# Optimization experiments

Hardware: AMD Instinct MI355X
Metric: run time of the kernel (lower is better)

Reference implementation:

```python
import jax, jax.numpy as jnp
import numpy as np

# Qwen3-0.6B-like config; 4 equal-length requests flattened into [R*S, H]
L, R, S, H = 2, 4, 1024, 1024
NH, NKV, DH = 16, 8, 128
FF = 3072
EPS = 1e-6
THETA = 1e6
SCALE = 0.02  # weight init scale to keep activations sane


def setup_inputs() -> dict:
    key = jax.random.key(0)
    ks = jax.random.split(key, 8)
    return {
        "hidden_states": jax.random.normal(ks[0], (R * S, H), jnp.float32),
        "Wq": jax.random.normal(ks[1], (L, H, NH * DH), jnp.float32) * SCALE,
        "Wk": jax.random.normal(ks[2], (L, H, NKV * DH), jnp.float32) * SCALE,
        "Wv": jax.random.normal(ks[3], (L, H, NKV * DH), jnp.float32) * SCALE,
        "Wo": jax.random.normal(ks[4], (L, NH * DH, H), jnp.float32) * SCALE,
        "q_norm_w": jnp.ones((L, DH), jnp.float32),
        "k_norm_w": jnp.ones((L, DH), jnp.float32),
        "ln1_w": jnp.ones((L, H), jnp.float32),
        "ln2_w": jnp.ones((L, H), jnp.float32),
        "Wg": jax.random.normal(ks[5], (L, H, FF), jnp.float32) * SCALE,
        "Wu": jax.random.normal(ks[6], (L, H, FF), jnp.float32) * SCALE,
        "Wd": jax.random.normal(ks[7], (L, FF, H), jnp.float32) * SCALE,
        "final_norm_w": jnp.ones((H,), jnp.float32),
    }


def _rms(x, w):
    return x * jax.lax.rsqrt(jnp.mean(x * x, axis=-1, keepdims=True) + EPS) * w


def _rope_tables():
    inv_freq = 1.0 / (THETA ** (jnp.arange(0, DH, 2, dtype=jnp.float32) / DH))
    pos = jnp.arange(S, dtype=jnp.float32)  # per-request positions 0..S-1 (prefill)
    freqs = pos[:, None] * inv_freq[None, :]        # [S, DH/2]
    emb = jnp.concatenate([freqs, freqs], axis=-1)  # [S, DH]
    return jnp.cos(emb), jnp.sin(emb)


def _rotate_half(x):
    x1, x2 = jnp.split(x, 2, axis=-1)
    return jnp.concatenate([-x2, x1], axis=-1)


def _apply_rope(x, cos, sin):
    # x: [R, heads, S, DH]; cos/sin: [S, DH]
    c = cos[None, None]
    s = sin[None, None]
    return x * c + _rotate_half(x) * s


def reference(hidden_states, Wq, Wk, Wv, Wo, q_norm_w, k_norm_w, ln1_w, ln2_w,
              Wg, Wu, Wd, final_norm_w):
    cos, sin = _rope_tables()
    causal = jnp.tril(jnp.ones((S, S), dtype=bool))  # per-request causal mask
    neg = jnp.finfo(hidden_states.dtype).min
    scaling = 1.0 / jnp.sqrt(jnp.asarray(DH, hidden_states.dtype))

    x = hidden_states
    for l in range(L):
        # --- attention block ---
        residual = x
        h = _rms(x, ln1_w[l])                       # [R*S, H]
        q = (h @ Wq[l]).reshape(R, S, NH, DH)
        k = (h @ Wk[l]).reshape(R, S, NKV, DH)
        v = (h @ Wv[l]).reshape(R, S, NKV, DH)
        q = _rms(q, q_norm_w[l]).transpose(0, 2, 1, 3)   # [R, NH, S, DH]
        k = _rms(k, k_norm_w[l]).transpose(0, 2, 1, 3)   # [R, NKV, S, DH]
        v = v.transpose(0, 2, 1, 3)                      # [R, NKV, S, DH]
        q = _apply_rope(q, cos, sin)
        k = _apply_rope(k, cos, sin)
        # GQA: repeat KV heads
        rep = NH // NKV
        k = jnp.repeat(k, rep, axis=1)
        v = jnp.repeat(v, rep, axis=1)
        scores = jnp.einsum('rhqd,rhkd->rhqk', q, k) * scaling
        scores = jnp.where(causal[None, None], scores, neg)
        attn = jax.nn.softmax(scores, axis=-1)
        o = jnp.einsum('rhqk,rhkd->rhqd', attn, v)       # [R, NH, S, DH]
        o = o.transpose(0, 2, 1, 3).reshape(R * S, NH * DH)
        x = residual + o @ Wo[l]
        # --- MLP block ---
        residual = x
        h = _rms(x, ln2_w[l])
        x = residual + (jax.nn.silu(h @ Wg[l]) * (h @ Wu[l])) @ Wd[l]
    return _rms(x, final_norm_w)
```

## Files before the change

### kernel.cpp

```cpp
#include <hip/hip_runtime.h>
#include <hip/hip_bf16.h>

typedef __bf16 bf16;
typedef __bf16 bf16x8 __attribute__((ext_vector_type(8)));
typedef float f32x4 __attribute__((ext_vector_type(4)));

#define DEVINL __device__ __forceinline__
#define SBAR() asm volatile("s_barrier" ::: "memory")

constexpr int L_ = 2, R_ = 4, S_ = 1024, H_ = 1024;
constexpr int NH_ = 16, NKV_ = 8, DH_ = 128;
constexpr int FF_ = 3072;
constexpr int T_ = R_ * S_;

DEVINL void gload16(const bf16* g, bf16* l) {
    __builtin_amdgcn_global_load_lds(
        (const __attribute__((address_space(1))) void*)g,
        (__attribute__((address_space(3))) void*)l, 16, 0, 0);
}

__global__ void rope_tables_kernel(float* __restrict__ cosb, float* __restrict__ sinb) {
    int s = blockIdx.x;
    int i = threadIdx.x;
    float inv = __expf(-(float)i * (1.0f / 64.0f) * 13.815510557964274f);
    float f = (float)s * inv;
    cosb[s * 64 + i] = cosf(f);
    sinb[s * 64 + i] = sinf(f);
}

template <bool OUT_BF16>
__global__ __launch_bounds__(256) void rmsnorm_kernel(const float* __restrict__ x,
                                                      const float* __restrict__ w,
                                                      void* __restrict__ out) {
    int row = blockIdx.x;
    const float* xr = x + (size_t)row * H_;
    int t = threadIdx.x;
    float v[4];
    float ss = 0.f;
#pragma unroll
    for (int j = 0; j < 4; ++j) {
        v[j] = xr[t + 256 * j];
        ss += v[j] * v[j];
    }
#pragma unroll
    for (int off = 32; off; off >>= 1) ss += __shfl_xor(ss, off);
    __shared__ float part[4];
    if ((t & 63) == 0) part[t >> 6] = ss;
    __syncthreads();
    ss = part[0] + part[1] + part[2] + part[3];
    float r = rsqrtf(ss * (1.0f / (float)H_) + 1e-6f);
#pragma unroll
    for (int j = 0; j < 4; ++j) {
        int c = t + 256 * j;
        float o = v[j] * r * w[c];
        if constexpr (OUT_BF16)
            ((bf16*)out)[(size_t)row * H_ + c] = (bf16)o;
        else
            ((float*)out)[(size_t)row * H_ + c] = o;
    }
}

__global__ __launch_bounds__(256) void transpose_all_kernel(
    const float* __restrict__ Wq, const float* __restrict__ Wk, const float* __restrict__ Wv,
    const float* __restrict__ Wo, const float* __restrict__ Wg, const float* __restrict__ Wu,
    const float* __restrict__ Wd, bf16* __restrict__ wqkv_t, bf16* __restrict__ wo_t,
    bf16* __restrict__ wgu_t, bf16* __restrict__ wd_t) {
    __shared__ float tile[32][33];
    int bid = blockIdx.x;
    const float* in;
    bf16* out;
    int Rk, Cn, mode, tid;
    if (bid < 2048) { in = Wq; out = wqkv_t; Rk = 1024; Cn = 2048; mode = 0; tid = bid; }
    else if (bid < 3072) { in = Wk; out = wqkv_t + (size_t)2048 * 1024; Rk = 1024; Cn = 1024; mode = 0; tid = bid - 2048; }
    else if (bid < 4096) { in = Wv; out = wqkv_t + (size_t)3072 * 1024; Rk = 1024; Cn = 1024; mode = 0; tid = bid - 3072; }
    else if (bid < 6144) { in = Wo; out = wo_t; Rk = 2048; Cn = 1024; mode = 0; tid = bid - 4096; }
    else if (bid < 9216) { in = Wg; out = wgu_t; Rk = 1024; Cn = 3072; mode = 1; tid = bid - 6144; }
    else if (bid < 12288) { in = Wu; out = wgu_t; Rk = 1024; Cn = 3072; mode = 2; tid = bid - 9216; }
    else { in = Wd; out = wd_t; Rk = 3072; Cn = 1024; mode = 0; tid = bid - 12288; }
    int nbx = Cn >> 5;
    int c0 = (tid % nbx) * 32, r0 = (tid / nbx) * 32;
    int t = threadIdx.x;
    int tc = t & 31, tr = t >> 5;
#pragma unroll
    for (int i = 0; i < 4; ++i) {
        int r = tr + i * 8;
        tile[r][tc] = in[(size_t)(r0 + r) * Cn + c0 + tc];
    }
    __syncthreads();
#pragma unroll
    for (int i = 0; i < 4; ++i) {
        int c = c0 + tr + i * 8;
        int n = (mode == 0) ? c : (((c >> 4) << 5) + ((mode == 2) ? 16 : 0) + (c & 15));
        out[(size_t)n * Rk + r0 + tc] = (bf16)tile[tc][tr + i * 8];
    }
}

__global__ __launch_bounds__(256) void vt_kernel(const bf16* __restrict__ qkv,
                                                 bf16* __restrict__ vt) {
    __shared__ bf16 tile[32][34];
    int s0 = blockIdx.x * 32, c0 = blockIdx.y * 32, r = blockIdx.z;
    int t = threadIdx.x, tc = t & 31, tr = t >> 5;
#pragma unroll
    for (int i = 0; i < 4; ++i) {
        int s = tr + i * 8;
        tile[s][tc] = qkv[(size_t)(r * 1024 + s0 + s) * 4096 + 3072 + c0 + tc];
    }
    __syncthreads();
#pragma unroll
    for (int i = 0; i < 4; ++i) {
        int c = tr + i * 8;
        vt[((size_t)(r * 1024 + c0 + c)) * 1024 + s0 + tc] = tile[tc][c];
    }
}

template <int EPI>
__global__ __launch_bounds__(512, 2) void gemmQ_kernel(const bf16* __restrict__ A,
                                                       const bf16* __restrict__ Bt,
                                                       void* __restrict__ out,
                                                       int M, int N, int K) {
    __shared__ bf16 lds[49152];
    const int NT = K >> 5;
    int nbm = M >> 8, nbn = N >> 8;
    int slice = nbn >> 3;
    int id = blockIdx.x;
    int xcd = id & 7, wi = id >> 3;
    int bm = (wi % nbm) << 8, bn = (xcd * slice + wi / nbm) << 8;
    int t = threadIdx.x, lane = t & 63, w = t >> 6;
    int wm = w >> 2, wn = w & 3;
    int hi = lane >> 4, f = lane & 15;

    int srow = t >> 2;
    int ssc = (t & 3) ^ ((srow >> 1) & 3);
    const bf16* a0 = A + (size_t)(bm + srow) * K + (ssc << 3);
    const bf16* a1 = A + (size_t)(bm + 128 + srow) * K + (ssc << 3);
    const bf16* b0 = Bt + (size_t)(bn + srow) * K + (ssc << 3);
    const bf16* b1 = Bt + (size_t)(bn + 128 + srow) * K + (ssc << 3);

    f32x4 acc[8][4] = {};

    gload16(a0, lds + 0 * 8192 + w * 512);
    gload16(a1, lds + 0 * 8192 + 4096 + w * 512);
    gload16(b0, lds + 24576 + 0 * 8192 + w * 512);
    gload16(b1, lds + 24576 + 0 * 8192 + 4096 + w * 512);
    gload16(a0 + 32, lds + 1 * 8192 + w * 512);
    gload16(a1 + 32, lds + 1 * 8192 + 4096 + w * 512);
    gload16(b0 + 32, lds + 24576 + 1 * 8192 + w * 512);
    gload16(b1 + 32, lds + 24576 + 1 * 8192 + 4096 + w * 512);
    asm volatile("s_waitcnt vmcnt(4)" ::: "memory");
    SBAR();

    int cb = 0;
    for (int tau = 0; tau < NT; ++tau) {
        const bf16* aB = lds + cb * 8192;
        const bf16* bB = lds + 24576 + cb * 8192;
        int sb = (cb == 0) ? 2 : cb - 1;
        bool doStage = (tau + 2 < NT);
        int tt = tau + 2;

        bf16x8 af[4], bfv[4];
#pragma unroll
        for (int mf = 0; mf < 4; ++mf) {
            int row = wm * 128 + mf * 16 + f;
            af[mf] = *(const bf16x8*)(aB + row * 32 + ((hi ^ ((row >> 1) & 3)) << 3));
        }
#pragma unroll
        for (int nf = 0; nf < 4; ++nf) {
            int row = wn * 64 + nf * 16 + f;
            bfv[nf] = *(const bf16x8*)(bB + row * 32 + ((hi ^ ((row >> 1) & 3)) << 3));
        }
        if (doStage) {
            gload16(a0 + tt * 32, lds + sb * 8192 + w * 512);
            gload16(a1 + tt * 32, lds + sb * 8192 + 4096 + w * 512);
        }
        SBAR();
        __builtin_amdgcn_s_setprio(1);
#pragma unroll
        for (int mf = 0; mf < 4; ++mf)
#pragma unroll
            for (int nf = 0; nf < 4; ++nf)
                acc[mf][nf] = __builtin_amdgcn_mfma_f32_16x16x32_bf16(af[mf], bfv[nf],
                                                                      acc[mf][nf], 0, 0, 0);
        __builtin_amdgcn_s_setprio(0);
        SBAR();

        bf16x8 af2[4];
#pragma unroll
        for (int mf = 0; mf < 4; ++mf) {
            int row = wm * 128 + (mf + 4) * 16 + f;
            af2[mf] = *(const bf16x8*)(aB + row * 32 + ((hi ^ ((row >> 1) & 3)) << 3));
        }
        if (doStage) {
            gload16(b0 + tt * 32, lds + 24576 + sb * 8192 + w * 512);
            gload16(b1 + tt * 32, lds + 24576 + sb * 8192 + 4096 + w * 512);
        }
        SBAR();
        __builtin_amdgcn_s_setprio(1);
#pragma unroll
        for (int mf = 0; mf < 4; ++mf)
#pragma unroll
            for (int nf = 0; nf < 4; ++nf)
                acc[mf + 4][nf] = __builtin_amdgcn_mfma_f32_16x16x32_bf16(af2[mf], bfv[nf],
                                                                          acc[mf + 4][nf], 0, 0, 0);
        __builtin_amdgcn_s_setprio(0);
        if (tau < NT - 2)
            asm volatile("s_waitcnt vmcnt(4)" ::: "memory");
        else
            asm volatile("s_waitcnt vmcnt(0)" ::: "memory");
        SBAR();
        cb = (cb == 2) ? 0 : cb + 1;
    }

    int rb = bm + wm * 128 + hi * 4;
#pragma unroll
    for (int mf = 0; mf < 8; ++mf) {
        if constexpr (EPI == 5) {
#pragma unroll
            for (int p = 0; p < 2; ++p) {
                int col = ((bn + wn * 64) >> 1) + p * 16 + f;
#pragma unroll
                for (int g = 0; g < 4; ++g) {
                    float gv = acc[mf][2 * p][g], uv = acc[mf][2 * p + 1][g];
                    float sv = gv / (1.0f + __expf(-gv));
                    ((bf16*)out)[(size_t)(rb + mf * 16 + g) * (N / 2) + col] = (bf16)(sv * uv);
                }
            }
        } else {
            int cb2 = bn + wn * 64 + f;
#pragma unroll
            for (int nf = 0; nf < 4; ++nf)
#pragma unroll
                for (int g = 0; g < 4; ++g)
                    ((bf16*)out)[(size_t)(rb + mf * 16 + g) * N + cb2 + nf * 16] =
                        (bf16)acc[mf][nf][g];
        }
    }
}

template <int EPI>
__global__ __launch_bounds__(256, 2) void gemmD_kernel(const bf16* __restrict__ A,
                                                       const bf16* __restrict__ Bt,
                                                       void* __restrict__ out,
                                                       const float* __restrict__ res,
                                                       int M, int N, int K) {
    __shared__ bf16 lds[36864];
    const int NT = K >> 6;
    int nbm = M >> 6;
    int id = blockIdx.x;
    int xcd = id & 7, wi = id >> 3;
    int bm = (wi % nbm) << 6, bn = xcd << 7;
    int t = threadIdx.x, lane = t & 63, w = t >> 6;
    int wm = w >> 1, wn = w & 1;
    int hi = lane >> 4, f = lane & 15;

    int ar0 = t >> 3, ac0 = t & 7;
    const bf16* aS0 = A + (size_t)(bm + ar0) * K + (((ac0 ^ (ar0 & 7)) & 7) << 3);
    const bf16* aS1 = A + (size_t)(bm + 32 + ar0) * K + (((ac0 ^ ((ar0 + 32) & 7)) & 7) << 3);
    const bf16* bS[4];
#pragma unroll
    for (int j = 0; j < 4; ++j) {
        int row = j * 32 + ar0;
        bS[j] = Bt + (size_t)(bn + row) * K + (((ac0 ^ (row & 7)) & 7) << 3);
    }

    f32x4 acc[2][4] = {};

    auto stage = [&](int tt, int sb) {
        gload16(aS0 + tt * 64, lds + sb * 4096 + w * 512);
        gload16(aS1 + tt * 64, lds + sb * 4096 + 2048 + w * 512);
#pragma unroll
        for (int j = 0; j < 4; ++j)
            gload16(bS[j] + tt * 64, lds + 12288 + sb * 8192 + j * 2048 + w * 512);
    };

    stage(0, 0);
    stage(1, 1);
    asm volatile("s_waitcnt vmcnt(6)" ::: "memory");
    __builtin_amdgcn_s_barrier();

    int cb = 0;
    for (int tau = 0; tau < NT; ++tau) {
        const bf16* aB = lds + cb * 4096;
        const bf16* bB = lds + 12288 + cb * 8192;
        if (tau + 2 < NT) stage(tau + 2, (cb == 0) ? 2 : cb - 1);
        bf16x8 af[2][2], bfv[2][4];
#pragma unroll
        for (int kh = 0; kh < 2; ++kh) {
            int q = kh * 4 + hi;
#pragma unroll
            for (int mf = 0; mf < 2; ++mf) {
                int row = wm * 32 + mf * 16 + f;
                af[kh][mf] = *(const bf16x8*)(aB + row * 64 + ((q ^ (row & 7)) << 3));
            }
#pragma unroll
            for (int nf = 0; nf < 4; ++nf) {
                int row = wn * 64 + nf * 16 + f;
                bfv[kh][nf] = *(const bf16x8*)(bB + row * 64 + ((q ^ (row & 7)) << 3));
            }
        }
        __builtin_amdgcn_s_setprio(1);
#pragma unroll
        for (int kh = 0; kh < 2; ++kh)
#pragma unroll
            for (int mf = 0; mf < 2; ++mf)
#pragma unroll
                for (int nf = 0; nf < 4; ++nf)
                    acc[mf][nf] = __builtin_amdgcn_mfma_f32_16x16x32_bf16(
                        af[kh][mf], bfv[kh][nf], acc[mf][nf], 0, 0, 0);
        __builtin_amdgcn_s_setprio(0);
        if (tau < NT - 2)
            asm volatile("s_waitcnt vmcnt(6)" ::: "memory");
        else
            asm volatile("s_waitcnt vmcnt(0)" ::: "memory");
        __builtin_amdgcn_s_barrier();
        cb = (cb == 2) ? 0 : cb + 1;
    }

    int rb = bm + wm * 32 + hi * 4;
    int cb2 = bn + wn * 64 + f;
#pragma unroll
    for (int mf = 0; mf < 2; ++mf)
#pragma unroll
        for (int nf = 0; nf < 4; ++nf)
#pragma unroll
            for (int g = 0; g < 4; ++g) {
                size_t idx = (size_t)(rb + mf * 16 + g) * N + cb2 + nf * 16;
                ((float*)out)[idx] = acc[mf][nf][g] + res[idx];
            }
}

DEVINL void head_norm_rope(const bf16* __restrict__ src, const float* __restrict__ w,
                           const float* __restrict__ cosb, const float* __restrict__ sinb,
                           int s, int ln, bf16* __restrict__ dst) {
    float x0 = (float)src[ln], x1 = (float)src[ln + 32];
    float x2 = (float)src[ln + 64], x3 = (float)src[ln + 96];
    float ss = x0 * x0 + x1 * x1 + x2 * x2 + x3 * x3;
#pragma unroll
    for (int off = 16; off; off >>= 1) ss += __shfl_xor(ss, off);
    float rr = rsqrtf(ss * (1.0f / 128.0f) + 1e-6f);
    float n0 = x0 * rr * w[ln], n1 = x1 * rr * w[ln + 32];
    float n2 = x2 * rr * w[ln + 64], n3 = x3 * rr * w[ln + 96];
    float c0 = cosb[s * 64 + ln], c1 = cosb[s * 64 + ln + 32];
    float s0 = sinb[s * 64 + ln], s1 = sinb[s * 64 + ln + 32];
    dst[ln] = (bf16)(n0 * c0 - n2 * s0);
    dst[ln + 32] = (bf16)(n1 * c1 - n3 * s1);
    dst[ln + 64] = (bf16)(n2 * c0 + n0 * s0);
    dst[ln + 96] = (bf16)(n3 * c1 + n1 * s1);
}

__global__ __launch_bounds__(256) void qkv_post_kernel(const bf16* __restrict__ qkv,
                                                       const float* __restrict__ qw,
                                                       const float* __restrict__ kw,
                                                       const float* __restrict__ cosb,
                                                       const float* __restrict__ sinb,
                                                       bf16* __restrict__ qo,
                                                       bf16* __restrict__ ko) {
    int tok = blockIdx.x;
    int r = tok >> 10, s = tok & 1023;
    int t = threadIdx.x;
    int g = t >> 5;
    int ln = t & 31;
    const bf16* row = qkv + (size_t)tok * 4096;
#pragma unroll
    for (int hh = 0; hh < 2; ++hh) {
        int h = g + hh * 8;
        head_norm_rope(row + h * 128, qw, cosb, sinb, s, ln,
                       qo + ((size_t)(r * NH_ + h) * S_ + s) * 128);
    }
    head_norm_rope(row + 2048 + g * 128, kw, cosb, sinb, s, ln,
                   ko + ((size_t)(r * NKV_ + g) * S_ + s) * 128);
}

__global__ __launch_bounds__(256, 2) void flash_kernel(const bf16* __restrict__ q,
                                                       const bf16* __restrict__ k,
                                                       const bf16* __restrict__ vt,
                                                       bf16* __restrict__ out) {
    __shared__ bf16 Kl[64 * 128];
    __shared__ bf16 Vl[128 * 64];
    __shared__ bf16 Pl[4][32][72];
    int bid = blockIdx.x;
    int grp = bid & 63, slot = bid >> 6;
    int strip = (slot < 4) ? (7 - slot) : (slot - 4);
    int h = 2 * (grp & 7) + ((grp >> 3) & 1);
    int r = grp >> 4;
    int kvh = h >> 1;

    int t = threadIdx.x, lane = t & 63, w = t >> 6;
    int arow = lane & 15, hi = lane >> 4;
    int a7 = arow & 7;
    int grow = hi * 4;
    int qbase = strip * 128 + w * 32;

    const bf16* qp = q + ((size_t)(r * NH_ + h) * S_ + qbase) * 128;
    bf16x8 qf[2][4];
#pragma unroll
    for (int m = 0; m < 2; ++m)
#pragma unroll
        for (int kc = 0; kc < 4; ++kc)
            qf[m][kc] = *(const bf16x8*)(qp + (size_t)(m * 16 + arow) * 128 + kc * 32 + hi * 8);

    const bf16* kp = k + (size_t)(r * NKV_ + kvh) * S_ * 128;
    const bf16* vp = vt + (size_t)(r * NKV_ + kvh) * 128 * S_;

    int krow0 = t >> 4, kc16 = t & 15;
    int vrow0 = t >> 3, vc16 = t & 7;

    f32x4 ao[2][8] = {};
    float mrow[2][4], lrow[2][4];
#pragma unroll
    for (int m = 0; m < 2; ++m)
#pragma unroll
        for (int g = 0; g < 4; ++g) { mrow[m][g] = -1e30f; lrow[m][g] = 0.f; }
    const float scale = 0.08838834764831845f;

    int nt = 2 * (strip + 1);
    bf16x8 krs[4], vrs[4];
#pragma unroll
    for (int i = 0; i < 4; ++i)
        krs[i] = *(const bf16x8*)(kp + (size_t)(krow0 + 16 * i) * 128 + kc16 * 8);
#pragma unroll
    for (int i = 0; i < 4; ++i)
        vrs[i] = *(const bf16x8*)(vp + (size_t)(vrow0 + 32 * i) * S_ + vc16 * 8);

    for (int it = 0; it < nt; ++it) {
        int kv0 = it * 64;
        __syncthreads();
#pragma unroll
        for (int i = 0; i < 4; ++i) {
            int row = krow0 + 16 * i;
            *(bf16x8*)(&Kl[row * 128 + ((kc16 ^ (row & 7)) * 8)]) = krs[i];
        }
#pragma unroll
        for (int i = 0; i < 4; ++i) {
            int row = vrow0 + 32 * i;
            *(bf16x8*)(&Vl[row * 64 + ((vc16 ^ (row & 7)) * 8)]) = vrs[i];
        }
        __syncthreads();
        if (it + 1 < nt) {
            int kvn = kv0 + 64;
#pragma unroll
            for (int i = 0; i < 4; ++i)
                krs[i] = *(const bf16x8*)(kp + (size_t)(kvn + krow0 + 16 * i) * 128 + kc16 * 8);
#pragma unroll
            for (int i = 0; i < 4; ++i)
                vrs[i] = *(const bf16x8*)(vp + (size_t)(vrow0 + 32 * i) * S_ + kvn + vc16 * 8);
        }
        f32x4 sc[2][4];
#pragma unroll
        for (int m = 0; m < 2; ++m)
#pragma unroll
            for (int n = 0; n < 4; ++n) sc[m][n] = (f32x4){0.f, 0.f, 0.f, 0.f};
#pragma unroll
        for (int n = 0; n < 4; ++n) {
            int krw = n * 16 + arow;
#pragma unroll
            for (int kc = 0; kc < 4; ++kc) {
                bf16x8 kf = *(const bf16x8*)(&Kl[krw * 128 + (((kc * 4 + hi) ^ a7) * 8)]);
                sc[0][n] = __builtin_amdgcn_mfma_f32_16x16x32_bf16(qf[0][kc], kf, sc[0][n], 0, 0, 0);
                sc[1][n] = __builtin_amdgcn_mfma_f32_16x16x32_bf16(qf[1][kc], kf, sc[1][n], 0, 0, 0);
            }
        }
#pragma unroll
        for (int m = 0; m < 2; ++m) {
            float pm[4][4];
            bool msk = (kv0 + 64 > qbase + m * 16);
#pragma unroll
            for (int n = 0; n < 4; ++n)
#pragma unroll
                for (int g = 0; g < 4; ++g) {
                    float sval = sc[m][n][g] * scale;
                    if (msk && (kv0 + n * 16 + arow > qbase + m * 16 + grow + g)) sval = -1e30f;
                    pm[n][g] = sval;
                }
            float mx[4], sf[4], rs[4];
#pragma unroll
            for (int g = 0; g < 4; ++g)
                mx[g] = fmaxf(fmaxf(pm[0][g], pm[1][g]), fmaxf(pm[2][g], pm[3][g]));
#pragma unroll
            for (int off = 8; off; off >>= 1)
#pragma unroll
                for (int g = 0; g < 4; ++g) mx[g] = fmaxf(mx[g], __shfl_xor(mx[g], off));
#pragma unroll
            for (int g = 0; g < 4; ++g) {
                float mnew = fmaxf(mrow[m][g], mx[g]);
                sf[g] = __expf(mrow[m][g] - mnew);
                mrow[m][g] = mnew;
            }
#pragma unroll
            for (int n = 0; n < 4; ++n)
#pragma unroll
                for (int g = 0; g < 4; ++g) pm[n][g] = __expf(pm[n][g] - mrow[m][g]);
#pragma unroll
            for (int g = 0; g < 4; ++g) rs[g] = pm[0][g] + pm[1][g] + pm[2][g] + pm[3][g];
#pragma unroll
            for (int off = 8; off; off >>= 1)
#pragma unroll
                for (int g = 0; g < 4; ++g) rs[g] += __shfl_xor(rs[g], off);
#pragma unroll
            for (int g = 0; g < 4; ++g) lrow[m][g] = lrow[m][g] * sf[g] + rs[g];
#pragma unroll
            for (int c = 0; c < 8; ++c)
#pragma unroll
                for (int g = 0; g < 4; ++g) ao[m][c][g] *= sf[g];
#pragma unroll
            for (int n = 0; n < 4; ++n)
#pragma unroll
                for (int g = 0; g < 4; ++g)
                    Pl[w][m * 16 + grow + g][n * 16 + arow] = (bf16)pm[n][g];
        }
        bf16x8 pf[2][2];
#pragma unroll
        for (int m = 0; m < 2; ++m)
#pragma unroll
            for (int ks = 0; ks < 2; ++ks)
                pf[m][ks] = *(const bf16x8*)(&Pl[w][m * 16 + arow][ks * 32 + hi * 8]);
#pragma unroll
        for (int c = 0; c < 8; ++c) {
            int vrw = c * 16 + arow;
#pragma unroll
            for (int ks = 0; ks < 2; ++ks) {
                bf16x8 vf = *(const bf16x8*)(&Vl[vrw * 64 + (((ks * 4 + hi) ^ a7) * 8)]);
                ao[0][c] = __builtin_amdgcn_mfma_f32_16x16x32_bf16(pf[0][ks], vf, ao[0][c], 0, 0, 0);
                ao[1][c] = __builtin_amdgcn_mfma_f32_16x16x32_bf16(pf[1][ks], vf, ao[1][c], 0, 0, 0);
            }
        }
    }
#pragma unroll
    for (int m = 0; m < 2; ++m)
#pragma unroll
        for (int c = 0; c < 8; ++c)
#pragma unroll
            for (int g = 0; g < 4; ++g) {
                int rq = qbase + m * 16 + grow + g;
                out[(size_t)(r * S_ + rq) * 2048 + h * 128 + c * 16 + arow] =
                    (bf16)(ao[m][c][g] / lrow[m][g]);
            }
}

extern "C" void kernel_launch(void* const* d_in, const int* in_sizes, int n_in,
                              void* d_out, int out_size, void* d_ws, size_t ws_size,
                              hipStream_t stream) {
    const float* hidden = (const float*)d_in[0];
    const float* Wq = (const float*)d_in[1];
    const float* Wk = (const float*)d_in[2];
    const float* Wv = (const float*)d_in[3];
    const float* Wo = (const float*)d_in[4];
    const float* qnw = (const float*)d_in[5];
    const float* knw = (const float*)d_in[6];
    const float* ln1 = (const float*)d_in[7];
    const float* ln2 = (const float*)d_in[8];
    const float* Wg = (const float*)d_in[9];
    const float* Wu = (const float*)d_in[10];
    const float* Wd = (const float*)d_in[11];
    const float* fnw = (const float*)d_in[12];
    float* out = (float*)d_out;

    char* ws = (char*)d_ws;
    size_t off = 0;
    auto alloc = [&](size_t bytes) -> char* {
        char* p = ws + off;
        off += (bytes + 255) & ~(size_t)255;
        return p;
    };
    float* cosb = (float*)alloc((size_t)S_ * 64 * 4);
    float* sinb = (float*)alloc((size_t)S_ * 64 * 4);
    float* x_ws = (float*)alloc((size_t)T_ * H_ * 4);
    bf16* hbuf = (bf16*)alloc((size_t)T_ * H_ * 2);
    bf16* qkv = (bf16*)alloc((size_t)T_ * 4096 * 2);
    bf16* act = qkv;
    bf16* qb = (bf16*)alloc((size_t)R_ * NH_ * S_ * 128 * 2);
    bf16* kb = (bf16*)alloc((size_t)R_ * NKV_ * S_ * 128 * 2);
    bf16* vtb = (bf16*)alloc((size_t)R_ * NKV_ * 128 * S_ * 2);
    bf16* attn = (bf16*)alloc((size_t)T_ * 2048 * 2);
    bf16* wqkv_t = (bf16*)alloc((size_t)4096 * 1024 * 2);
    bf16* wo_t = (bf16*)alloc((size_t)1024 * 2048 * 2);
    bf16* wgu_t = (bf16*)alloc((size_t)6144 * 1024 * 2);
    bf16* wd_t = (bf16*)alloc((size_t)1024 * 3072 * 2);

    rope_tables_kernel<<<S_, 64, 0, stream>>>(cosb, sinb);

    const float* xin = hidden;
    for (int l = 0; l < L_; ++l) {
        transpose_all_kernel<<<15360, 256, 0, stream>>>(
            Wq + (size_t)l * H_ * 2048, Wk + (size_t)l * H_ * 1024, Wv + (size_t)l * H_ * 1024,
            Wo + (size_t)l * 2048 * 1024, Wg + (size_t)l * H_ * 3072, Wu + (size_t)l * H_ * 3072,
            Wd + (size_t)l * 3072 * 1024, wqkv_t, wo_t, wgu_t, wd_t);

        rmsnorm_kernel<true><<<T_, 256, 0, stream>>>(xin, ln1 + (size_t)l * H_, hbuf);
        gemmQ_kernel<1><<<256, 512, 0, stream>>>(hbuf, wqkv_t, qkv, 4096, 4096, 1024);
        qkv_post_kernel<<<T_, 256, 0, stream>>>(qkv, qnw + (size_t)l * 128, knw + (size_t)l * 128,
                                                cosb, sinb, qb, kb);
        vt_kernel<<<dim3(32, 32, 4), 256, 0, stream>>>(qkv, vtb);
        flash_kernel<<<512, 256, 0, stream>>>(qb, kb, vtb, attn);
        gemmD_kernel<4><<<512, 256, 0, stream>>>(attn, wo_t, x_ws, xin, 4096, 1024, 2048);
        rmsnorm_kernel<true><<<T_, 256, 0, stream>>>(x_ws, ln2 + (size_t)l * H_, hbuf);
        gemmQ_kernel<5><<<384, 512, 0, stream>>>(hbuf, wgu_t, act, 4096, 6144, 1024);
        gemmD_kernel<4><<<512, 256, 0, stream>>>(act, wd_t, x_ws, x_ws, 4096, 1024, 3072);
        xin = x_ws;
    }
    rmsnorm_kernel<false><<<T_, 256, 0, stream>>>(x_ws, fnw, out);
}
```

Before: 552.0 us.

## Halve GEMM M-tile to 128 rows and simplify pipelined loop barriers

Replaces the 256x256-tile QKV and gate/up GEMM with a 128x256 tile, doubling grid size and raising launch bounds to four blocks per CU. The K-loop now issues all stage loads at the top of each iteration and keeps only one barrier per step instead of three. This aims to improve occupancy and latency hiding and to cut barrier overhead. The trade-off is lower data reuse per block and more global traffic for B.

```diff
diff --git a/kernel.cpp b/kernel.cpp
--- a/kernel.cpp
+++ b/kernel.cpp
@@ -6,7 +6,6 @@
 typedef float f32x4 __attribute__((ext_vector_type(4)));
 
 #define DEVINL __device__ __forceinline__
-#define SBAR() asm volatile("s_barrier" ::: "memory")
 
 constexpr int L_ = 2, R_ = 4, S_ = 1024, H_ = 1024;
 constexpr int NH_ = 16, NKV_ = 8, DH_ = 128;
@@ -114,53 +113,49 @@
 }
 
 template <int EPI>
-__global__ __launch_bounds__(512, 2) void gemmQ_kernel(const bf16* __restrict__ A,
+__global__ __launch_bounds__(512, 4) void gemmP_kernel(const bf16* __restrict__ A,
                                                        const bf16* __restrict__ Bt,
                                                        void* __restrict__ out,
                                                        int M, int N, int K) {
-    __shared__ bf16 lds[49152];
+    __shared__ bf16 lds[36864];
     const int NT = K >> 5;
-    int nbm = M >> 8, nbn = N >> 8;
+    int nbm = M >> 7, nbn = N >> 8;
     int slice = nbn >> 3;
     int id = blockIdx.x;
     int xcd = id & 7, wi = id >> 3;
-    int bm = (wi % nbm) << 8, bn = (xcd * slice + wi / nbm) << 8;
+    int bm = (wi % nbm) << 7, bn = (xcd * slice + wi / nbm) << 8;
     int t = threadIdx.x, lane = t & 63, w = t >> 6;
     int wm = w >> 2, wn = w & 3;
     int hi = lane >> 4, f = lane & 15;
 
     int srow = t >> 2;
     int ssc = (t & 3) ^ ((srow >> 1) & 3);
-    const bf16* a0 = A + (size_t)(bm + srow) * K + (ssc << 3);
-    const bf16* a1 = A + (size_t)(bm + 128 + srow) * K + (ssc << 3);
-    const bf16* b0 = Bt + (size_t)(bn + srow) * K + (ssc << 3);
-    const bf16* b1 = Bt + (size_t)(bn + 128 + srow) * K + (ssc << 3);
-
-    f32x4 acc[8][4] = {};
-
-    gload16(a0, lds + 0 * 8192 + w * 512);
-    gload16(a1, lds + 0 * 8192 + 4096 + w * 512);
-    gload16(b0, lds + 24576 + 0 * 8192 + w * 512);
-    gload16(b1, lds + 24576 + 0 * 8192 + 4096 + w * 512);
-    gload16(a0 + 32, lds + 1 * 8192 + w * 512);
-    gload16(a1 + 32, lds + 1 * 8192 + 4096 + w * 512);
-    gload16(b0 + 32, lds + 24576 + 1 * 8192 + w * 512);
-    gload16(b1 + 32, lds + 24576 + 1 * 8192 + 4096 + w * 512);
-    asm volatile("s_waitcnt vmcnt(4)" ::: "memory");
-    SBAR();
+    const bf16* aSrc = A + (size_t)(bm + srow) * K + (ssc << 3);
+    const bf16* b0Src = Bt + (size_t)(bn + srow) * K + (ssc << 3);
+    const bf16* b1Src = Bt + (size_t)(bn + 128 + srow) * K + (ssc << 3);
+
+    f32x4 acc[4][4] = {};
+
+    auto stage = [&](int tt, int sb) {
+        gload16(aSrc + tt * 32, lds + sb * 4096 + w * 512);
+        gload16(b0Src + tt * 32, lds + 12288 + sb * 8192 + w * 512);
+        gload16(b1Src + tt * 32, lds + 12288 + sb * 8192 + 4096 + w * 512);
+    };
+
+    stage(0, 0);
+    stage(1, 1);
+    asm volatile("s_waitcnt vmcnt(3)" ::: "memory");
+    __builtin_amdgcn_s_barrier();
 
     int cb = 0;
     for (int tau = 0; tau < NT; ++tau) {
-        const bf16* aB = lds + cb * 8192;
-        const bf16* bB = lds + 24576 + cb * 8192;
-        int sb = (cb == 0) ? 2 : cb - 1;
-        bool doStage = (tau + 2 < NT);
-        int tt = tau + 2;
-
+        const bf16* aB = lds + cb * 4096;
+        const bf16* bB = lds + 12288 + cb * 8192;
+        if (tau + 2 < NT) stage(tau + 2, (cb == 0) ? 2 : cb - 1);
         bf16x8 af[4], bfv[4];
 #pragma unroll
         for (int mf = 0; mf < 4; ++mf) {
-            int row = wm * 128 + mf * 16 + f;
+            int row = wm * 64 + mf * 16 + f;
             af[mf] = *(const bf16x8*)(aB + row * 32 + ((hi ^ ((row >> 1) & 3)) << 3));
         }
 #pragma unroll
@@ -168,11 +163,6 @@
             int row = wn * 64 + nf * 16 + f;
             bfv[nf] = *(const bf16x8*)(bB + row * 32 + ((hi ^ ((row >> 1) & 3)) << 3));
         }
-        if (doStage) {
-            gload16(a0 + tt * 32, lds + sb * 8192 + w * 512);
-            gload16(a1 + tt * 32, lds + sb * 8192 + 4096 + w * 512);
-        }
-        SBAR();
         __builtin_amdgcn_s_setprio(1);
 #pragma unroll
         for (int mf = 0; mf < 4; ++mf)
@@ -181,38 +171,17 @@
                 acc[mf][nf] = __builtin_amdgcn_mfma_f32_16x16x32_bf16(af[mf], bfv[nf],
                                                                       acc[mf][nf], 0, 0, 0);
         __builtin_amdgcn_s_setprio(0);
-        SBAR();
-
-        bf16x8 af2[4];
-#pragma unroll
-        for (int mf = 0; mf < 4; ++mf) {
-            int row = wm * 128 + (mf + 4) * 16 + f;
-            af2[mf] = *(const bf16x8*)(aB + row * 32 + ((hi ^ ((row >> 1) & 3)) << 3));
-        }
-        if (doStage) {
-            gload16(b0 + tt * 32, lds + 24576 + sb * 8192 + w * 512);
-            gload16(b1 + tt * 32, lds + 24576 + sb * 8192 + 4096 + w * 512);
-        }
-        SBAR();
-        __builtin_amdgcn_s_setprio(1);
-#pragma unroll
-        for (int mf = 0; mf < 4; ++mf)
-#pragma unroll
-            for (int nf = 0; nf < 4; ++nf)
-                acc[mf + 4][nf] = __builtin_amdgcn_mfma_f32_16x16x32_bf16(af2[mf], bfv[nf],
-                                                                          acc[mf + 4][nf], 0, 0, 0);
-        __builtin_amdgcn_s_setprio(0);
         if (tau < NT - 2)
-            asm volatile("s_waitcnt vmcnt(4)" ::: "memory");
+            asm volatile("s_waitcnt vmcnt(3)" ::: "memory");
         else
             asm volatile("s_waitcnt vmcnt(0)" ::: "memory");
-        SBAR();
+        __builtin_amdgcn_s_barrier();
         cb = (cb == 2) ? 0 : cb + 1;
     }
 
-    int rb = bm + wm * 128 + hi * 4;
-#pragma unroll
-    for (int mf = 0; mf < 8; ++mf) {
+    int rb = bm + wm * 64 + hi * 4;
+#pragma unroll
+    for (int mf = 0; mf < 4; ++mf) {
         if constexpr (EPI == 5) {
 #pragma unroll
             for (int p = 0; p < 2; ++p) {
@@ -586,14 +555,14 @@
             Wd + (size_t)l * 3072 * 1024, wqkv_t, wo_t, wgu_t, wd_t);
 
         rmsnorm_kernel<true><<<T_, 256, 0, stream>>>(xin, ln1 + (size_t)l * H_, hbuf);
-        gemmQ_kernel<1><<<256, 512, 0, stream>>>(hbuf, wqkv_t, qkv, 4096, 4096, 1024);
+        gemmP_kernel<1><<<512, 512, 0, stream>>>(hbuf, wqkv_t, qkv, 4096, 4096, 1024);
         qkv_post_kernel<<<T_, 256, 0, stream>>>(qkv, qnw + (size_t)l * 128, knw + (size_t)l * 128,
                                                 cosb, sinb, qb, kb);
         vt_kernel<<<dim3(32, 32, 4), 256, 0, stream>>>(qkv, vtb);
         flash_kernel<<<512, 256, 0, stream>>>(qb, kb, vtb, attn);
         gemmD_kernel<4><<<512, 256, 0, stream>>>(attn, wo_t, x_ws, xin, 4096, 1024, 2048);
         rmsnorm_kernel<true><<<T_, 256, 0, stream>>>(x_ws, ln2 + (size_t)l * H_, hbuf);
-        gemmQ_kernel<5><<<384, 512, 0, stream>>>(hbuf, wgu_t, act, 4096, 6144, 1024);
+        gemmP_kernel<5><<<768, 512, 0, stream>>>(hbuf, wgu_t, act, 4096, 6144, 1024);
         gemmD_kernel<4><<<512, 256, 0, stream>>>(act, wd_t, x_ws, x_ws, 4096, 1024, 3072);
         xin = x_ws;
     }
```

New measurement: 531.3 us. 3.8% less time.
